# Kernel optimization log

Hardware: AMD Instinct MI355X
Metric: run time of the kernel (lower is better)

Reference implementation:

```python
import jax, jax.numpy as jnp
import numpy as np

K, M_EMB, N_HID, D_CTX, D_ATT, M_COV = 128, 256, 256, 684, 512, 256
B, H, W = 64, 16, 48


def gru_cell(x, h, W_ih, W_hh, b_ih, b_hh):
    # PyTorch GRUCell semantics
    gi = x @ W_ih.T + b_ih
    gh = h @ W_hh.T + b_hh
    i_r, i_z, i_n = jnp.split(gi, 3, axis=-1)
    h_r, h_z, h_n = jnp.split(gh, 3, axis=-1)
    r = jax.nn.sigmoid(i_r + h_r)
    z = jax.nn.sigmoid(i_z + h_z)
    n = jnp.tanh(i_n + r * h_n)
    return (1.0 - z) * n + z * h


def setup_inputs() -> dict:
    key = jax.random.key(0)
    ks = jax.random.split(key, 24)
    s = 0.02
    inp = {
        'y': jax.random.randint(ks[0], (B,), 0, K),
        'y_mask': jnp.ones((B,), jnp.float32),
        'context': jax.random.normal(ks[1], (B, D_CTX, H, W), jnp.float32),
        'pre_hidden': jax.random.normal(ks[2], (B, N_HID), jnp.float32),
        'alpha_past': jax.random.uniform(ks[3], (B, H, W), jnp.float32),
        'emb': jax.random.normal(ks[4], (K + 1, M_EMB)) * s,
        'W_ih1': jax.random.normal(ks[5], (3 * N_HID, M_EMB)) * s,
        'W_hh1': jax.random.normal(ks[6], (3 * N_HID, N_HID)) * s,
        'b_ih1': jnp.zeros((3 * N_HID,)),
        'b_hh1': jnp.zeros((3 * N_HID,)),
        'conv_Ua_w': jax.random.normal(ks[7], (D_ATT, D_CTX, 1, 1)) * s,
        'conv_Ua_b': jnp.zeros((D_ATT,)),
        'Wa': jax.random.normal(ks[8], (D_ATT, N_HID)) * s,
        'conv_Q_w': jax.random.normal(ks[9], (M_COV, 1, 3, 3)) * s,
        'Uf': jax.random.normal(ks[10], (D_ATT, M_COV)) * s,
        'Uf_b': jnp.zeros((D_ATT,)),
        'va': jax.random.normal(ks[11], (1, D_ATT)) * s,
        'va_b': jnp.zeros((1,)),
        'W_ih2': jax.random.normal(ks[12], (3 * N_HID, D_CTX)) * s,
        'W_hh2': jax.random.normal(ks[13], (3 * N_HID, N_HID)) * s,
        'b_ih2': jnp.zeros((3 * N_HID,)),
        'b_hh2': jnp.zeros((3 * N_HID,)),
        'Wct': jax.random.normal(ks[14], (M_EMB, D_CTX)) * s,
        'Wct_b': jnp.zeros((M_EMB,)),
        'Wht': jax.random.normal(ks[15], (M_EMB, N_HID)) * s,
        'Wht_b': jnp.zeros((M_EMB,)),
        'W0': jax.random.normal(ks[16], (K, M_EMB // 2)) * s,
        'W0_b': jnp.zeros((K,)),
    }
    return inp


def reference(y, y_mask, context, pre_hidden, alpha_past, emb,
              W_ih1, W_hh1, b_ih1, b_hh1, conv_Ua_w, conv_Ua_b, Wa,
              conv_Q_w, Uf, Uf_b, va, va_b,
              W_ih2, W_hh2, b_ih2, b_hh2, Wct, Wct_b, Wht, Wht_b, W0, W0_b):
    embedded = emb[y]                                           # [B, m]
    s_hat = gru_cell(embedded, pre_hidden, W_ih1, W_hh1, b_ih1, b_hh1)
    s_hat = y_mask[:, None] * s_hat + (1.0 - y_mask)[:, None] * pre_hidden

    Wa_h1 = s_hat @ Wa.T                                        # [B, A]
    # 1x1 conv == channel projection, output in NHWC layout
    Ua_ctx = jnp.einsum('bdhw,ad->bhwa', context, conv_Ua_w[:, :, 0, 0]) + conv_Ua_b
    # 3x3 coverage conv over past attention map
    cover_F = jax.lax.conv_general_dilated(
        alpha_past[:, None, :, :], conv_Q_w, (1, 1), 'SAME',
        dimension_numbers=('NCHW', 'OIHW', 'NCHW'))              # [B, M, H, W]
    cover_F = jnp.transpose(cover_F, (0, 2, 3, 1))               # [B, H, W, M]
    cover_vector = cover_F @ Uf.T + Uf_b                         # [B, H, W, A]

    e_att = jnp.tanh(Ua_ctx + Wa_h1[:, None, None, :] + cover_vector)
    alpha = (e_att @ va.T + va_b)[..., 0].reshape(e_att.shape[0], -1)  # [B, H*W]
    alpha = jax.nn.softmax(alpha, axis=1)

    ct = jnp.einsum('bdp,bp->bd', context.reshape(context.shape[0], context.shape[1], -1), alpha)

    s = gru_cell(ct, s_hat, W_ih2, W_hh2, b_ih2, b_hh2)
    s = y_mask[:, None] * s + (1.0 - y_mask)[:, None] * s_hat

    logit = ct @ Wct.T + Wct_b + s @ Wht.T + Wht_b + embedded    # [B, m]
    logit = logit.reshape(logit.shape[0], -1, 2).max(axis=2)     # maxout -> [B, m/2]
    out = logit @ W0.T + W0_b                                    # [B, K]
    return out, s, alpha.reshape(alpha.shape[0], H, W)
```

## Files before the change

### kernel.cpp

```cpp
#include <hip/hip_runtime.h>
#include <hip/hip_bf16.h>
#include <math.h>

#define BB 64
#define KV 128
#define ME 256
#define NH 256
#define DC 684
#define DA 512
#define MC 256
#define HH_ 16
#define WW_ 48
#define HW_ 768
#define NS 22

typedef __attribute__((ext_vector_type(8))) short bf16x8;
typedef __attribute__((ext_vector_type(4))) float f32x4;

#define WS_G     0
#define WS_RB    (WS_G + 4608)
#define WS_EMB   (WS_RB + 32768)
#define WS_SH    (WS_EMB + 16384)
#define WS_AL    (WS_SH + 16384)
#define WS_CT    (WS_AL + 49152)
#define WS_APACK (WS_CT + 43776)
#define WS_GI    (WS_APACK + 180224)
#define WS_GH    (WS_GI + 49152)
#define WS_LG    WS_GI
#define WS_BP    (WS_GH + 49152)
#define NEED_BYTES ((size_t)441600 * 4 + (size_t)34603008 * 2)

static __device__ __forceinline__ unsigned short f2b(float v) {
    __hip_bfloat16 h = __float2bfloat16(v);
    return *reinterpret_cast<unsigned short*>(&h);
}

template <int AUX>
static __device__ __forceinline__ void gl_lds16(const unsigned short* g,
                                                unsigned short* l) {
    __builtin_amdgcn_global_load_lds(
        (const __attribute__((address_space(1))) unsigned int*)g,
        (__attribute__((address_space(3))) unsigned int*)l, 16, 0, AUX);
}

__global__ __launch_bounds__(512) void k_prep(
    const float* __restrict__ ctx, const float* __restrict__ Ua,
    const float* __restrict__ Uf, const float* __restrict__ convQ,
    const int* __restrict__ y, const float* __restrict__ emb,
    unsigned short* __restrict__ Bpack, unsigned short* __restrict__ Apack,
    float* __restrict__ G, float* __restrict__ embedded) {
    __shared__ unsigned short Ts[64 * 360];
    int bx = blockIdx.x, t = threadIdx.x;
    if (bx < 768) {
        int b = bx / 12, pt = bx % 12, p0 = pt * 64;
        int w = t >> 6, p = t & 63;
        unsigned short* dst = Bpack + (long)(b * 12 + pt) * 22 * 2048;
        for (int ch = 0; ch < 2; ch++) {
            int dbase = ch * 352;
            if (ch) __syncthreads();
#pragma unroll
            for (int iter = 0; iter < 11; iter++) {
                int d0 = dbase + iter * 32 + w * 4;
                float v0 = 0.f, v1 = 0.f, v2 = 0.f, v3 = 0.f;
                const float* src = ctx + ((long)b * DC + d0) * HW_ + p0 + p;
                if (d0 + 0 < DC) v0 = src[0];
                if (d0 + 1 < DC) v1 = src[HW_];
                if (d0 + 2 < DC) v2 = src[2 * HW_];
                if (d0 + 3 < DC) v3 = src[3 * HW_];
                unsigned u01 = (unsigned)f2b(v0) | ((unsigned)f2b(v1) << 16);
                unsigned u23 = (unsigned)f2b(v2) | ((unsigned)f2b(v3) << 16);
                *(uint2*)&Ts[p * 360 + (d0 - dbase)] = make_uint2(u01, u23);
            }
            __syncthreads();
            int so = t >> 8;
            int tt = t & 255;
            int pp = tt >> 2, slot = tt & 3;
#pragma unroll
            for (int s2 = 0; s2 < 12; s2 += 2) {
                int sl = s2 + so;
                if (sl < 11) {
                    int s = ch * 11 + sl;
                    bf16x8 v = *(const bf16x8*)&Ts[pp * 360 + sl * 32 +
                                                   ((slot ^ ((pp >> 1) & 3))
                                                    << 3)];
                    *(bf16x8*)(dst + (long)(s * 256 + tt) * 8) = v;
                }
            }
        }
    } else if (bx < 856) {
        int bi = bx - 768;
#pragma unroll
        for (int r = 0; r < 8; r++) {
            int idx = bi * 4096 + r * 512 + t;
            int e = idx & 7, slot = (idx >> 3) & 3;
            int a = (idx >> 5) & 511, s = idx >> 14;
            int d = s * 32 + ((slot ^ ((a >> 1) & 3)) << 3) + e;
            float v = (d < DC) ? Ua[a * DC + d] : 0.f;
            Apack[idx] = f2b(v);
        }
    } else if (bx < 865) {
        int idx = (bx - 856) * 512 + t;
        if (idx < DA * 9) {
            int a = idx / 9, k = idx % 9;
            float s = 0.f;
            for (int m = 0; m < MC; m++) s += Uf[a * MC + m] * convQ[m * 9 + k];
            G[idx] = s;
        }
    } else {
        int b = bx - 865;
        if (t < ME) embedded[b * ME + t] = emb[y[b] * ME + t];
    }
}

__global__ __launch_bounds__(256) void k_G(const float* __restrict__ Uf,
                                           const float* __restrict__ convQ,
                                           float* __restrict__ G) {
    int idx = blockIdx.x * 256 + threadIdx.x;
    if (idx >= DA * 9) return;
    int a = idx / 9, k = idx % 9;
    float s = 0.f;
    for (int m = 0; m < MC; m++) s += Uf[a * MC + m] * convQ[m * 9 + k];
    G[idx] = s;
}

__global__ __launch_bounds__(256) void k_prepA(const float* __restrict__ Ua,
                                               unsigned short* __restrict__ Apack) {
    int idx = blockIdx.x * 256 + threadIdx.x;
    if (idx >= NS * DA * 32) return;
    int e = idx & 7, slot = (idx >> 3) & 3;
    int a = (idx >> 5) & 511, s = idx >> 14;
    int d = s * 32 + ((slot ^ ((a >> 1) & 3)) << 3) + e;
    float v = (d < DC) ? Ua[a * DC + d] : 0.f;
    Apack[idx] = f2b(v);
}

__global__ __launch_bounds__(256) void k_emb(const int* __restrict__ y,
                                             const float* __restrict__ emb,
                                             float* __restrict__ embedded) {
    int b = blockIdx.x, t = threadIdx.x;
    embedded[b * ME + t] = emb[y[b] * ME + t];
}

__global__ __launch_bounds__(256) void k_rows256(
    const float* __restrict__ X, const float* __restrict__ W,
    const float* __restrict__ bias, const float* __restrict__ bias2,
    float* __restrict__ out, int outStride) {
    __shared__ float Xs[64 * 257];
    __shared__ float Ws[4 * 260];
    int t = threadIdx.x, w = t >> 6, lane = t & 63;
    for (int i = t; i < 64 * 256; i += 256) {
        int bb = i >> 8, k = i & 255;
        Xs[bb * 257 + k] = X[bb * 256 + k];
    }
    int r = blockIdx.x * 4 + w;
    *(f32x4*)(Ws + w * 260 + lane * 4) = *(const f32x4*)(W + r * 256 + lane * 4);
    __syncthreads();
    const float* xrow = Xs + lane * 257;
    const float* wrow = Ws + w * 260;
    float acc = 0.f;
#pragma unroll 8
    for (int k = 0; k < 256; k++) acc += wrow[k] * xrow[k];
    acc += bias[r];
    if (bias2) acc += bias2[r];
    out[lane * outStride + r] = acc;
}

__global__ __launch_bounds__(256) void k_gih1(
    const float* __restrict__ embedded, const float* __restrict__ pre_hidden,
    const float* __restrict__ W_ih1, const float* __restrict__ W_hh1,
    const float* __restrict__ b_ih1, const float* __restrict__ b_hh1,
    float* __restrict__ gi, float* __restrict__ gh) {
    __shared__ float Xs[64 * 257];
    __shared__ float Ws[4 * 260];
    int bx = blockIdx.x, t = threadIdx.x, w = t >> 6, lane = t & 63;
    const float *X, *W, *bias;
    float* outp;
    int r;
    if (bx < 192) {
        X = embedded; W = W_ih1; bias = b_ih1; outp = gi; r = bx * 4 + w;
    } else {
        X = pre_hidden; W = W_hh1; bias = b_hh1; outp = gh; r = (bx - 192) * 4 + w;
    }
    for (int i = t; i < 64 * 256; i += 256) {
        int bb = i >> 8, k = i & 255;
        Xs[bb * 257 + k] = X[bb * 256 + k];
    }
    *(f32x4*)(Ws + w * 260 + lane * 4) = *(const f32x4*)(W + r * 256 + lane * 4);
    __syncthreads();
    const float* xrow = Xs + lane * 257;
    const float* wrow = Ws + w * 260;
    float acc = 0.f;
#pragma unroll 8
    for (int k = 0; k < 256; k++) acc += wrow[k] * xrow[k];
    outp[lane * 768 + r] = acc + bias[r];
}

__global__ __launch_bounds__(256) void k_gih2(
    const float* __restrict__ ctv, const float* __restrict__ s_hat,
    const float* __restrict__ W_ih2, const float* __restrict__ W_hh2,
    const float* __restrict__ b_ih2, const float* __restrict__ b_hh2,
    float* __restrict__ gi, float* __restrict__ gh) {
    __shared__ float Xs[64 * 257];
    __shared__ float Ws[4 * 260];
    int bx = blockIdx.x, t = threadIdx.x, w = t >> 6, lane = t & 63;
    if (bx < 192) {
        int r = bx * 4 + w;
        float acc = 0.f;
        for (int c = 0; c < 3; c++) {
            int c0 = c * 228;
            __syncthreads();
            for (int i = t; i < 64 * 228; i += 256) {
                int bb = i / 228, kk = i - bb * 228;
                Xs[bb * 229 + kk] = ctv[bb * DC + c0 + kk];
            }
            for (int j = lane; j < 228; j += 64)
                Ws[w * 260 + j] = W_ih2[r * DC + c0 + j];
            __syncthreads();
            const float* xrow = Xs + lane * 229;
            const float* wrow = Ws + w * 260;
#pragma unroll 4
            for (int k = 0; k < 228; k++) acc += wrow[k] * xrow[k];
        }
        gi[lane * 768 + r] = acc + b_ih2[r];
    } else {
        int r = (bx - 192) * 4 + w;
        for (int i = t; i < 64 * 256; i += 256) {
            int bb = i >> 8, k = i & 255;
            Xs[bb * 257 + k] = s_hat[bb * 256 + k];
        }
        *(f32x4*)(Ws + w * 260 + lane * 4) =
            *(const f32x4*)(W_hh2 + r * 256 + lane * 4);
        __syncthreads();
        const float* xrow = Xs + lane * 257;
        const float* wrow = Ws + w * 260;
        float acc = 0.f;
#pragma unroll 8
        for (int k = 0; k < 256; k++) acc += wrow[k] * xrow[k];
        gh[lane * 768 + r] = acc + b_hh2[r];
    }
}

__global__ __launch_bounds__(256) void k_gru(const float* __restrict__ gi,
                                             const float* __restrict__ gh,
                                             const float* __restrict__ h,
                                             const float* __restrict__ y_mask,
                                             float* __restrict__ outp) {
    int b = blockIdx.x, t = threadIdx.x;
    float hv = h[b * NH + t];
    float r = 1.f / (1.f + expf(-(gi[b * 768 + t] + gh[b * 768 + t])));
    float z = 1.f / (1.f + expf(-(gi[b * 768 + 256 + t] + gh[b * 768 + 256 + t])));
    float n = tanhf(gi[b * 768 + 512 + t] + r * gh[b * 768 + 512 + t]);
    float sv = (1.f - z) * n + z * hv;
    float m = y_mask[b];
    outp[b * NH + t] = m * sv + (1.f - m) * hv;
}

__global__ __launch_bounds__(512) void k_att_cnt(
    const unsigned short* __restrict__ Apack,
    const unsigned short* __restrict__ Bpack, const float* __restrict__ G,
    const float* __restrict__ rb, const float* __restrict__ va,
    const float* __restrict__ va_b, const float* __restrict__ apast,
    float* __restrict__ alogit) {
    __shared__ __attribute__((aligned(16))) unsigned short lsA[2][16384];
    __shared__ __attribute__((aligned(16))) unsigned short lsB[2][2048];
    __shared__ float ap_s[18 * 50];
    __shared__ float part_s[8][64];
    int pt = blockIdx.x, b = blockIdx.y;
    int t = threadIdx.x, w = t >> 6, lane = t & 63;
    int l15 = lane & 15, lg = lane >> 4;
    int sx = lg ^ ((l15 >> 1) & 3);

    for (int idx = t; idx < 900; idx += 512) {
        int hh = idx / 50, ww = idx % 50;
        float v = 0.f;
        if (hh >= 1 && hh <= HH_ && ww >= 1 && ww <= WW_)
            v = apast[b * HW_ + (hh - 1) * WW_ + (ww - 1)];
        ap_s[idx] = v;
    }
    __syncthreads();

    const unsigned short* Asrc = Apack + w * 2048 + lane * 8;
    const unsigned short* Bsrc =
        Bpack + (long)(b * 12 + pt) * 22 * 2048 + (w & 3) * 512 + lane * 8;

#define STAGE(S, BUF)                                                        \
    do {                                                                     \
        _Pragma("unroll") for (int i_ = 0; i_ < 4; i_++)                     \
            gl_lds16<0>(Asrc + (long)(S)*16384 + i_ * 512,                   \
                        &lsA[BUF][w * 2048 + i_ * 512]);                     \
        gl_lds16<2>(Bsrc + (long)(S)*2048, &lsB[BUF][(w & 3) * 512]);        \
    } while (0)

#define STEP_BODY(CUR)                                                       \
    do {                                                                     \
        bf16x8 af[4], bf[4];                                                 \
        _Pragma("unroll") for (int j = 0; j < 4; j++)                        \
            bf[j] = *(const bf16x8*)&lsB[CUR][(j * 16 + l15) * 32 + sx * 8]; \
        _Pragma("unroll") for (int i = 0; i < 4; i++)                        \
            af[i] = *(const bf16x8*)&lsA[CUR][(w * 64 + i * 16 + l15) * 32 + \
                                             sx * 8];                        \
        _Pragma("unroll") for (int i = 0; i < 4; i++)                        \
            _Pragma("unroll") for (int j = 0; j < 4; j++)                    \
                acc[i][j] = __builtin_amdgcn_mfma_f32_16x16x32_bf16(         \
                    af[i], bf[j], acc[i][j], 0, 0, 0);                       \
    } while (0)

    f32x4 acc[4][4];
#pragma unroll
    for (int i = 0; i < 4; i++)
#pragma unroll
        for (int j = 0; j < 4; j++) acc[i][j] = {0.f, 0.f, 0.f, 0.f};

    STAGE(0, 0);
    STAGE(1, 1);

    for (int s = 0; s < NS - 1; s++) {
        int cur = s & 1;
        asm volatile("s_waitcnt vmcnt(5)" ::: "memory");
        __builtin_amdgcn_sched_barrier(0);
        __builtin_amdgcn_s_barrier();
        __builtin_amdgcn_sched_barrier(0);
        STEP_BODY(cur);
        __builtin_amdgcn_s_barrier();
        __builtin_amdgcn_sched_barrier(0);
        if (s + 2 < NS) STAGE(s + 2, cur);
    }
    asm volatile("s_waitcnt vmcnt(0)" ::: "memory");
    __builtin_amdgcn_sched_barrier(0);
    __builtin_amdgcn_s_barrier();
    __builtin_amdgcn_sched_barrier(0);
    STEP_BODY((NS - 1) & 1);
#undef STAGE
#undef STEP_BODY

    float partial[4] = {0.f, 0.f, 0.f, 0.f};
#pragma unroll
    for (int i = 0; i < 4; i++) {
#pragma unroll
        for (int r = 0; r < 4; r++) {
            int a = w * 64 + i * 16 + lg * 4 + r;
            float rbv = rb[b * DA + a];
            float vav = va[a];
            const float* Ga = G + a * 9;
            float g0 = Ga[0], g1 = Ga[1], g2 = Ga[2], g3 = Ga[3], g4 = Ga[4];
            float g5 = Ga[5], g6 = Ga[6], g7 = Ga[7], g8 = Ga[8];
#pragma unroll
            for (int j = 0; j < 4; j++) {
                int p = pt * 64 + j * 16 + l15;
                int hh = p / WW_, ww = p % WW_;
                const float* ap = ap_s + hh * 50 + ww;
                float cov = g0 * ap[0] + g1 * ap[1] + g2 * ap[2] +
                            g3 * ap[50] + g4 * ap[51] + g5 * ap[52] +
                            g6 * ap[100] + g7 * ap[101] + g8 * ap[102];
                float e = tanhf(acc[i][j][r] + rbv + cov);
                partial[j] += vav * e;
            }
        }
    }
#pragma unroll
    for (int j = 0; j < 4; j++) {
        partial[j] += __shfl_xor(partial[j], 16);
        partial[j] += __shfl_xor(partial[j], 32);
    }
    if (lane < 16) {
#pragma unroll
        for (int j = 0; j < 4; j++) part_s[w][j * 16 + lane] = partial[j];
    }
    __syncthreads();
    if (t < 64) {
        float sum = va_b[0];
#pragma unroll
        for (int q = 0; q < 8; q++) sum += part_s[q][t];
        alogit[b * HW_ + pt * 64 + t] = sum;
    }
}

#define LDW 40
__global__ __launch_bounds__(256) void k_att_lds(
    const unsigned short* __restrict__ Apack, const float* __restrict__ ctx,
    const float* __restrict__ G, const float* __restrict__ rb,
    const float* __restrict__ va, const float* __restrict__ va_b,
    const float* __restrict__ apast, float* __restrict__ alogit) {
    __shared__ __attribute__((aligned(16))) short lsB[2][64 * LDW];
    __shared__ float ap_s[18 * 50];
    __shared__ float part_s[4 * 64];
    int b = blockIdx.y;
    int p0 = blockIdx.x * 64;
    int t = threadIdx.x;
    int w = t >> 6, lane = t & 63;
    int l15 = lane & 15, lg = lane >> 4;
    int sxA = lg ^ ((l15 >> 1) & 3);
    int pq = t & 15, kp = t >> 4;
    const float* ctx_b = ctx + (long)b * DC * HW_ + p0;

    for (int idx = t; idx < 900; idx += 256) {
        int hh = idx / 50, ww = idx % 50;
        float v = 0.f;
        if (hh >= 1 && hh <= HH_ && ww >= 1 && ww <= WW_)
            v = apast[b * HW_ + (hh - 1) * WW_ + (ww - 1)];
        ap_s[idx] = v;
    }

#define CTXLOAD(FA, FB, S)                                                   \
    do {                                                                     \
        int d_ = (S) * 32 + 2 * kp;                                          \
        const float* s0_ = ctx_b + (long)d_ * HW_ + pq;                      \
        bool g0_ = d_ < DC, g1_ = (d_ + 1) < DC;                             \
        _Pragma("unroll") for (int j_ = 0; j_ < 4; j_++) {                   \
            FA[j_] = g0_ ? s0_[16 * j_] : 0.f;                               \
            FB[j_] = g1_ ? s0_[HW_ + 16 * j_] : 0.f;                         \
        }                                                                    \
    } while (0)
#define STAGEW(FA, FB, BUF)                                                  \
    do {                                                                     \
        _Pragma("unroll") for (int j_ = 0; j_ < 4; j_++) {                   \
            ((unsigned*)lsB[BUF])[(pq + 16 * j_) * (LDW / 2) + kp] =         \
                (unsigned)f2b(FA[j_]) | ((unsigned)f2b(FB[j_]) << 16);       \
        }                                                                    \
    } while (0)
#define ALOAD(AF, S)                                                         \
    do {                                                                     \
        _Pragma("unroll") for (int i_ = 0; i_ < 8; i_++)                     \
            AF[i_] = *(const bf16x8*)(Apack +                                \
                ((long)((S)*512 + w * 128 + i_ * 16 + l15) * 4 + sxA) * 8);  \
    } while (0)
#define BREAD(BF, BUF)                                                       \
    do {                                                                     \
        _Pragma("unroll") for (int j_ = 0; j_ < 4; j_++)                     \
            BF[j_] = *(const bf16x8*)(&lsB[BUF][(j_ * 16 + l15) * LDW +      \
                                               lg * 8]);                     \
    } while (0)
#define MFMA8x4(AF, BF)                                                      \
    do {                                                                     \
        _Pragma("unroll") for (int i_ = 0; i_ < 8; i_++)                     \
            _Pragma("unroll") for (int j_ = 0; j_ < 4; j_++)                 \
                acc[i_][j_] = __builtin_amdgcn_mfma_f32_16x16x32_bf16(       \
                    AF[i_], BF[j_], acc[i_][j_], 0, 0, 0);                   \
    } while (0)

    f32x4 acc[8][4];
#pragma unroll
    for (int i = 0; i < 8; i++)
#pragma unroll
        for (int j = 0; j < 4; j++) acc[i][j] = {0.f, 0.f, 0.f, 0.f};

    float fa0[4], fb0[4], fa1[4], fb1[4];
    bf16x8 afr0[8], afr1[8], bfr[4];

    CTXLOAD(fa1, fb1, 0);
    ALOAD(afr0, 0);
    STAGEW(fa1, fb1, 0);
    CTXLOAD(fa1, fb1, 1);
    __syncthreads();

    for (int ss = 0; ss < NS; ss += 2) {
        if (ss + 2 < NS) CTXLOAD(fa0, fb0, ss + 2);
        ALOAD(afr1, ss + 1);
        BREAD(bfr, 0);
        STAGEW(fa1, fb1, 1);
        MFMA8x4(afr0, bfr);
        __syncthreads();
        if (ss + 3 < NS) CTXLOAD(fa1, fb1, ss + 3);
        if (ss + 2 < NS) {
            ALOAD(afr0, ss + 2);
            BREAD(bfr, 1);
            STAGEW(fa0, fb0, 0);
            MFMA8x4(afr1, bfr);
        } else {
            BREAD(bfr, 1);
            MFMA8x4(afr1, bfr);
        }
        __syncthreads();
    }

    float partial[4] = {0.f, 0.f, 0.f, 0.f};
#pragma unroll
    for (int i = 0; i < 8; i++) {
#pragma unroll
        for (int r = 0; r < 4; r++) {
            int a = w * 128 + i * 16 + lg * 4 + r;
            float rbv = rb[b * DA + a];
            float vav = va[a];
            const float* Ga = G + a * 9;
            float g0 = Ga[0], g1 = Ga[1], g2 = Ga[2], g3 = Ga[3], g4 = Ga[4];
            float g5 = Ga[5], g6 = Ga[6], g7 = Ga[7], g8 = Ga[8];
#pragma unroll
            for (int j = 0; j < 4; j++) {
                int p = p0 + j * 16 + l15;
                int hh = p / WW_, ww = p % WW_;
                const float* ap = ap_s + hh * 50 + ww;
                float cov = g0 * ap[0] + g1 * ap[1] + g2 * ap[2] +
                            g3 * ap[50] + g4 * ap[51] + g5 * ap[52] +
                            g6 * ap[100] + g7 * ap[101] + g8 * ap[102];
                float e = tanhf(acc[i][j][r] + rbv + cov);
                partial[j] += vav * e;
            }
        }
    }
#pragma unroll
    for (int j = 0; j < 4; j++) {
        partial[j] += __shfl_xor(partial[j], 16);
        partial[j] += __shfl_xor(partial[j], 32);
    }
    if (lane < 16) {
#pragma unroll
        for (int j = 0; j < 4; j++) part_s[w * 64 + j * 16 + lane] = partial[j];
    }
    __syncthreads();
    if (t < 64) {
        float s = va_b[0] + part_s[t] + part_s[64 + t] + part_s[128 + t] +
                  part_s[192 + t];
        alogit[b * HW_ + p0 + t] = s;
    }
}

__global__ __launch_bounds__(256) void k_ctsm(const float* __restrict__ ctx,
                                              const float* __restrict__ alogit,
                                              float* __restrict__ ct,
                                              float* __restrict__ alpha_out) {
    __shared__ float al_s[HW_];
    __shared__ float red[16];
    int b = blockIdx.y, t = threadIdx.x;
    float v[3];
    float mx = -1e30f;
    for (int i = 0; i < 3; i++) {
        v[i] = alogit[b * HW_ + i * 256 + t];
        mx = fmaxf(mx, v[i]);
    }
    for (int off = 32; off > 0; off >>= 1) mx = fmaxf(mx, __shfl_down(mx, off));
    if ((t & 63) == 0) red[t >> 6] = mx;
    __syncthreads();
    if (t == 0) red[0] = fmaxf(fmaxf(red[0], red[1]), fmaxf(red[2], red[3]));
    __syncthreads();
    mx = red[0];
    float sum = 0.f;
    for (int i = 0; i < 3; i++) {
        v[i] = expf(v[i] - mx);
        sum += v[i];
    }
    for (int off = 32; off > 0; off >>= 1) sum += __shfl_down(sum, off);
    if ((t & 63) == 0) red[8 + (t >> 6)] = sum;
    __syncthreads();
    if (t == 0) red[8] = red[8] + red[9] + red[10] + red[11];
    __syncthreads();
    float inv = 1.f / red[8];
    for (int i = 0; i < 3; i++) {
        float a = v[i] * inv;
        al_s[i * 256 + t] = a;
        if (blockIdx.x == 0) alpha_out[b * HW_ + i * 256 + t] = a;
    }
    __syncthreads();
    int dc0 = blockIdx.x * 114;
    int wave = t >> 6, lane = t & 63;
    for (int d = dc0 + wave; d < dc0 + 114; d += 4) {
        const float* row = &ctx[((long)b * DC + d) * HW_];
        float s = 0.f;
#pragma unroll
        for (int q = 0; q < 12; q++) s += row[lane + q * 64] * al_s[lane + q * 64];
        for (int off = 32; off > 0; off >>= 1) s += __shfl_down(s, off);
        if (lane == 0) ct[b * DC + d] = s;
    }
}

__global__ __launch_bounds__(256) void k_logit(
    const float* __restrict__ ctv, const float* __restrict__ s,
    const float* __restrict__ embedded, const float* __restrict__ Wct,
    const float* __restrict__ Wht, const float* __restrict__ Wct_b,
    const float* __restrict__ Wht_b, float* __restrict__ lg) {
    __shared__ float Xs[64 * 257];
    __shared__ float Ws[4 * 232];
    int t = threadIdx.x, w = t >> 6, lane = t & 63;
    int r = blockIdx.x * 4 + w;
    float acc = 0.f;
    for (int c = 0; c < 3; c++) {
        int c0 = c * 228;
        __syncthreads();
        for (int i = t; i < 64 * 228; i += 256) {
            int bb = i / 228, kk = i - bb * 228;
            Xs[bb * 229 + kk] = ctv[bb * DC + c0 + kk];
        }
        for (int j = lane; j < 228; j += 64) Ws[w * 232 + j] = Wct[r * DC + c0 + j];
        __syncthreads();
        const float* xrow = Xs + lane * 229;
        const float* wrow = Ws + w * 232;
#pragma unroll 4
        for (int k = 0; k < 228; k++) acc += wrow[k] * xrow[k];
    }
    __syncthreads();
    for (int i = t; i < 64 * 256; i += 256) {
        int bb = i >> 8, k = i & 255;
        Xs[bb * 257 + k] = s[bb * 256 + k];
    }
    __syncthreads();
    const float* xrow2 = Xs + lane * 257;
    const float* wr = Wht + r * 256;
    float acc2 = 0.f;
#pragma unroll 8
    for (int k = 0; k < 256; k++) acc2 += wr[k] * xrow2[k];
    lg[lane * 256 + r] = acc + acc2 + Wct_b[r] + Wht_b[r] + embedded[lane * 256 + r];
}

__global__ __launch_bounds__(256) void k_head(const float* __restrict__ lg,
                                              const float* __restrict__ W0,
                                              const float* __restrict__ W0_b,
                                              float* __restrict__ out) {
    __shared__ float Xs[64 * 129];
    __shared__ float Ws[4 * 132];
    int t = threadIdx.x, w = t >> 6, lane = t & 63;
    for (int i = t; i < 64 * 128; i += 256) {
        int bb = i >> 7, m = i & 127;
        Xs[bb * 129 + m] = fmaxf(lg[bb * 256 + 2 * m], lg[bb * 256 + 2 * m + 1]);
    }
    int r = blockIdx.x * 4 + w;
    Ws[w * 132 + lane] = W0[r * 128 + lane];
    Ws[w * 132 + 64 + lane] = W0[r * 128 + 64 + lane];
    __syncthreads();
    const float* xrow = Xs + lane * 129;
    const float* wrow = Ws + w * 132;
    float acc = 0.f;
#pragma unroll 8
    for (int k = 0; k < 128; k++) acc += wrow[k] * xrow[k];
    out[lane * KV + r] = acc + W0_b[r];
}

extern "C" void kernel_launch(void* const* d_in, const int* in_sizes, int n_in,
                              void* d_out, int out_size, void* d_ws,
                              size_t ws_size, hipStream_t stream) {
    const int* y = (const int*)d_in[0];
    const float* y_mask = (const float*)d_in[1];
    const float* context = (const float*)d_in[2];
    const float* pre_hidden = (const float*)d_in[3];
    const float* alpha_past = (const float*)d_in[4];
    const float* emb = (const float*)d_in[5];
    const float* W_ih1 = (const float*)d_in[6];
    const float* W_hh1 = (const float*)d_in[7];
    const float* b_ih1 = (const float*)d_in[8];
    const float* b_hh1 = (const float*)d_in[9];
    const float* conv_Ua_w = (const float*)d_in[10];
    const float* conv_Ua_b = (const float*)d_in[11];
    const float* Wa = (const float*)d_in[12];
    const float* conv_Q_w = (const float*)d_in[13];
    const float* Uf = (const float*)d_in[14];
    const float* Uf_b = (const float*)d_in[15];
    const float* va = (const float*)d_in[16];
    const float* va_b = (const float*)d_in[17];
    const float* W_ih2 = (const float*)d_in[18];
    const float* W_hh2 = (const float*)d_in[19];
    const float* b_ih2 = (const float*)d_in[20];
    const float* b_hh2 = (const float*)d_in[21];
    const float* Wct = (const float*)d_in[22];
    const float* Wct_b = (const float*)d_in[23];
    const float* Wht = (const float*)d_in[24];
    const float* Wht_b = (const float*)d_in[25];
    const float* W0 = (const float*)d_in[26];
    const float* W0_b = (const float*)d_in[27];

    float* ws = (float*)d_ws;
    float* out = (float*)d_out;
    float* G = ws + WS_G;
    float* rbias = ws + WS_RB;
    float* embedded = ws + WS_EMB;
    float* s_hat = ws + WS_SH;
    float* alogit = ws + WS_AL;
    float* ctv = ws + WS_CT;
    unsigned short* Apack = (unsigned short*)(ws + WS_APACK);
    float* gi = ws + WS_GI;
    float* gh = ws + WS_GH;
    float* lg = ws + WS_LG;
    unsigned short* Bpack = (unsigned short*)(ws + WS_BP);
    float* s_out = out + 8192;
    float* alpha_out = out + 24576;

    bool fast = ws_size >= NEED_BYTES;

    if (fast) {
        k_prep<<<dim3(929), dim3(512), 0, stream>>>(context, conv_Ua_w, Uf,
                                                    conv_Q_w, y, emb, Bpack,
                                                    Apack, G, embedded);
    } else {
        k_G<<<dim3(18), dim3(256), 0, stream>>>(Uf, conv_Q_w, G);
        k_prepA<<<dim3((NS * DA * 32 + 255) / 256), dim3(256), 0, stream>>>(
            conv_Ua_w, Apack);
        k_emb<<<dim3(64), dim3(256), 0, stream>>>(y, emb, embedded);
    }
    k_gih1<<<dim3(384), dim3(256), 0, stream>>>(embedded, pre_hidden, W_ih1,
                                                W_hh1, b_ih1, b_hh1, gi, gh);
    k_gru<<<dim3(64), dim3(256), 0, stream>>>(gi, gh, pre_hidden, y_mask, s_hat);
    k_rows256<<<dim3(128), dim3(256), 0, stream>>>(s_hat, Wa, conv_Ua_b, Uf_b,
                                                   rbias, 512);
    if (fast) {
        k_att_cnt<<<dim3(12, 64), dim3(512), 0, stream>>>(
            Apack, Bpack, G, rbias, va, va_b, alpha_past, alogit);
    } else {
        k_att_lds<<<dim3(12, 64), dim3(256), 0, stream>>>(
            Apack, context, G, rbias, va, va_b, alpha_past, alogit);
    }
    k_ctsm<<<dim3(6, 64), dim3(256), 0, stream>>>(context, alogit, ctv,
                                                  alpha_out);
    k_gih2<<<dim3(384), dim3(256), 0, stream>>>(ctv, s_hat, W_ih2, W_hh2, b_ih2,
                                                b_hh2, gi, gh);
    k_gru<<<dim3(64), dim3(256), 0, stream>>>(gi, gh, s_hat, y_mask, s_out);
    k_logit<<<dim3(64), dim3(256), 0, stream>>>(ctv, s_out, embedded, Wct, Wht,
                                                Wct_b, Wht_b, lg);
    k_head<<<dim3(32), dim3(256), 0, stream>>>(lg, W0, W0_b, out);
}
```

Before: 247.6 us.

## Retile attention GEMM into 256x192 blocks split over attention-dim halves

The attention-energy kernel now tiles each block as half of the attention dimension (256) by 192 positions instead of all 512 by 64, so each wave computes a 64x96 output tile with six B fragments per step. This raises A-operand reuse across positions and cuts repeated loads of the packed Ua weights, at the cost of two partial logit buffers that the softmax kernel sums. The va_b bias is dropped because softmax is shift-invariant. The fallback path zeroes the second buffer with a memset, and the larger accumulator array raises register pressure.

```diff
diff --git a/kernel.cpp b/kernel.cpp
--- a/kernel.cpp
+++ b/kernel.cpp
@@ -28,7 +28,8 @@
 #define WS_GH    (WS_GI + 49152)
 #define WS_LG    WS_GI
 #define WS_BP    (WS_GH + 49152)
-#define NEED_BYTES ((size_t)441600 * 4 + (size_t)34603008 * 2)
+#define WS_AL2   (WS_BP + 17301504)
+#define NEED_BYTES ((size_t)(441600 + 17301504 + 49152) * 4)
 
 static __device__ __forceinline__ unsigned short f2b(float v) {
     __hip_bfloat16 h = __float2bfloat16(v);
@@ -255,19 +256,20 @@
     outp[b * NH + t] = m * sv + (1.f - m) * hv;
 }
 
-__global__ __launch_bounds__(512) void k_att_cnt(
+__global__ __launch_bounds__(512) void k_att3(
     const unsigned short* __restrict__ Apack,
     const unsigned short* __restrict__ Bpack, const float* __restrict__ G,
     const float* __restrict__ rb, const float* __restrict__ va,
-    const float* __restrict__ va_b, const float* __restrict__ apast,
-    float* __restrict__ alogit) {
-    __shared__ __attribute__((aligned(16))) unsigned short lsA[2][16384];
-    __shared__ __attribute__((aligned(16))) unsigned short lsB[2][2048];
+    const float* __restrict__ apast, float* __restrict__ alogit0,
+    float* __restrict__ alogit1) {
+    __shared__ __attribute__((aligned(16))) unsigned short lsA[2][8192];
+    __shared__ __attribute__((aligned(16))) unsigned short lsB[2][6144];
     __shared__ float ap_s[18 * 50];
-    __shared__ float part_s[8][64];
-    int pt = blockIdx.x, b = blockIdx.y;
+    __shared__ float part_s[8][96];
+    int pt = blockIdx.x, ah = blockIdx.y, b = blockIdx.z;
     int t = threadIdx.x, w = t >> 6, lane = t & 63;
     int l15 = lane & 15, lg = lane >> 4;
+    int aw = w & 3, pw = w >> 2;
     int sx = lg ^ ((l15 >> 1) & 3);
 
     for (int idx = t; idx < 900; idx += 512) {
@@ -279,44 +281,57 @@
     }
     __syncthreads();
 
-    const unsigned short* Asrc = Apack + w * 2048 + lane * 8;
-    const unsigned short* Bsrc =
-        Bpack + (long)(b * 12 + pt) * 22 * 2048 + (w & 3) * 512 + lane * 8;
+    const unsigned short* Ap0 = Apack + ah * 8192 + w * 1024 + lane * 8;
+    const unsigned short* Bp0[2];
+    int ldst[2];
+    {
+#pragma unroll
+        for (int i = 0; i < 2; i++) {
+            int l = w * 2 + i;
+            if (l >= 12) l -= 12;
+            int c = l >> 2, q = l & 3;
+            Bp0[i] = Bpack + (long)(b * 12 + pt * 3 + c) * 22 * 2048 + q * 512 +
+                     lane * 8;
+            ldst[i] = c * 2048 + q * 512;
+        }
+    }
 
 #define STAGE(S, BUF)                                                        \
     do {                                                                     \
-        _Pragma("unroll") for (int i_ = 0; i_ < 4; i_++)                     \
-            gl_lds16<0>(Asrc + (long)(S)*16384 + i_ * 512,                   \
-                        &lsA[BUF][w * 2048 + i_ * 512]);                     \
-        gl_lds16<2>(Bsrc + (long)(S)*2048, &lsB[BUF][(w & 3) * 512]);        \
+        _Pragma("unroll") for (int i_ = 0; i_ < 2; i_++)                     \
+            gl_lds16<0>(Ap0 + (long)(S)*16384 + i_ * 512,                    \
+                        &lsA[BUF][w * 1024 + i_ * 512]);                     \
+        _Pragma("unroll") for (int i_ = 0; i_ < 2; i_++)                     \
+            gl_lds16<2>(Bp0[i_] + (long)(S)*2048, &lsB[BUF][ldst[i_]]);      \
     } while (0)
 
 #define STEP_BODY(CUR)                                                       \
     do {                                                                     \
-        bf16x8 af[4], bf[4];                                                 \
-        _Pragma("unroll") for (int j = 0; j < 4; j++)                        \
-            bf[j] = *(const bf16x8*)&lsB[CUR][(j * 16 + l15) * 32 + sx * 8]; \
+        bf16x8 af[4], bf[6];                                                 \
         _Pragma("unroll") for (int i = 0; i < 4; i++)                        \
-            af[i] = *(const bf16x8*)&lsA[CUR][(w * 64 + i * 16 + l15) * 32 + \
+            af[i] = *(const bf16x8*)&lsA[CUR][(aw * 64 + i * 16 + l15) * 32 +\
+                                             sx * 8];                        \
+        _Pragma("unroll") for (int j = 0; j < 6; j++)                        \
+            bf[j] = *(const bf16x8*)&lsB[CUR][(pw * 96 + j * 16 + l15) * 32 +\
                                              sx * 8];                        \
         _Pragma("unroll") for (int i = 0; i < 4; i++)                        \
-            _Pragma("unroll") for (int j = 0; j < 4; j++)                    \
+            _Pragma("unroll") for (int j = 0; j < 6; j++)                    \
                 acc[i][j] = __builtin_amdgcn_mfma_f32_16x16x32_bf16(         \
                     af[i], bf[j], acc[i][j], 0, 0, 0);                       \
     } while (0)
 
-    f32x4 acc[4][4];
+    f32x4 acc[4][6];
 #pragma unroll
     for (int i = 0; i < 4; i++)
 #pragma unroll
-        for (int j = 0; j < 4; j++) acc[i][j] = {0.f, 0.f, 0.f, 0.f};
+        for (int j = 0; j < 6; j++) acc[i][j] = {0.f, 0.f, 0.f, 0.f};
 
     STAGE(0, 0);
     STAGE(1, 1);
 
     for (int s = 0; s < NS - 1; s++) {
         int cur = s & 1;
-        asm volatile("s_waitcnt vmcnt(5)" ::: "memory");
+        asm volatile("s_waitcnt vmcnt(4)" ::: "memory");
         __builtin_amdgcn_sched_barrier(0);
         __builtin_amdgcn_s_barrier();
         __builtin_amdgcn_sched_barrier(0);
@@ -333,20 +348,20 @@
 #undef STAGE
 #undef STEP_BODY
 
-    float partial[4] = {0.f, 0.f, 0.f, 0.f};
+    float partial[6] = {0.f, 0.f, 0.f, 0.f, 0.f, 0.f};
 #pragma unroll
     for (int i = 0; i < 4; i++) {
 #pragma unroll
         for (int r = 0; r < 4; r++) {
-            int a = w * 64 + i * 16 + lg * 4 + r;
+            int a = ah * 256 + aw * 64 + i * 16 + lg * 4 + r;
             float rbv = rb[b * DA + a];
             float vav = va[a];
             const float* Ga = G + a * 9;
             float g0 = Ga[0], g1 = Ga[1], g2 = Ga[2], g3 = Ga[3], g4 = Ga[4];
             float g5 = Ga[5], g6 = Ga[6], g7 = Ga[7], g8 = Ga[8];
 #pragma unroll
-            for (int j = 0; j < 4; j++) {
-                int p = pt * 64 + j * 16 + l15;
+            for (int j = 0; j < 6; j++) {
+                int p = pt * 192 + pw * 96 + j * 16 + l15;
                 int hh = p / WW_, ww = p % WW_;
                 const float* ap = ap_s + hh * 50 + ww;
                 float cov = g0 * ap[0] + g1 * ap[1] + g2 * ap[2] +
@@ -358,20 +373,21 @@
         }
     }
 #pragma unroll
-    for (int j = 0; j < 4; j++) {
+    for (int j = 0; j < 6; j++) {
         partial[j] += __shfl_xor(partial[j], 16);
         partial[j] += __shfl_xor(partial[j], 32);
     }
     if (lane < 16) {
 #pragma unroll
-        for (int j = 0; j < 4; j++) part_s[w][j * 16 + lane] = partial[j];
-    }
-    __syncthreads();
-    if (t < 64) {
-        float sum = va_b[0];
-#pragma unroll
-        for (int q = 0; q < 8; q++) sum += part_s[q][t];
-        alogit[b * HW_ + pt * 64 + t] = sum;
+        for (int j = 0; j < 6; j++) part_s[w][j * 16 + lane] = partial[j];
+    }
+    __syncthreads();
+    if (t < 192) {
+        int pg = t / 96, pl = t % 96;
+        float sum = part_s[pg * 4 + 0][pl] + part_s[pg * 4 + 1][pl] +
+                    part_s[pg * 4 + 2][pl] + part_s[pg * 4 + 3][pl];
+        float* dst = ah ? alogit1 : alogit0;
+        dst[b * HW_ + pt * 192 + t] = sum;
     }
 }
 
@@ -379,8 +395,8 @@
 __global__ __launch_bounds__(256) void k_att_lds(
     const unsigned short* __restrict__ Apack, const float* __restrict__ ctx,
     const float* __restrict__ G, const float* __restrict__ rb,
-    const float* __restrict__ va, const float* __restrict__ va_b,
-    const float* __restrict__ apast, float* __restrict__ alogit) {
+    const float* __restrict__ va, const float* __restrict__ apast,
+    float* __restrict__ alogit) {
     __shared__ __attribute__((aligned(16))) short lsB[2][64 * LDW];
     __shared__ float ap_s[18 * 50];
     __shared__ float part_s[4 * 64];
@@ -508,14 +524,15 @@
     }
     __syncthreads();
     if (t < 64) {
-        float s = va_b[0] + part_s[t] + part_s[64 + t] + part_s[128 + t] +
+        float s = part_s[t] + part_s[64 + t] + part_s[128 + t] +
                   part_s[192 + t];
         alogit[b * HW_ + p0 + t] = s;
     }
 }
 
 __global__ __launch_bounds__(256) void k_ctsm(const float* __restrict__ ctx,
-                                              const float* __restrict__ alogit,
+                                              const float* __restrict__ alogit0,
+                                              const float* __restrict__ alogit1,
                                               float* __restrict__ ct,
                                               float* __restrict__ alpha_out) {
     __shared__ float al_s[HW_];
@@ -524,7 +541,8 @@
     float v[3];
     float mx = -1e30f;
     for (int i = 0; i < 3; i++) {
-        v[i] = alogit[b * HW_ + i * 256 + t];
+        int idx = b * HW_ + i * 256 + t;
+        v[i] = alogit0[idx] + alogit1[idx];
         mx = fmaxf(mx, v[i]);
     }
     for (int off = 32; off > 0; off >>= 1) mx = fmaxf(mx, __shfl_down(mx, off));
@@ -668,6 +686,7 @@
     float* gh = ws + WS_GH;
     float* lg = ws + WS_LG;
     unsigned short* Bpack = (unsigned short*)(ws + WS_BP);
+    float* alogit2 = ws + WS_AL2;
     float* s_out = out + 8192;
     float* alpha_out = out + 24576;
 
@@ -682,6 +701,7 @@
         k_prepA<<<dim3((NS * DA * 32 + 255) / 256), dim3(256), 0, stream>>>(
             conv_Ua_w, Apack);
         k_emb<<<dim3(64), dim3(256), 0, stream>>>(y, emb, embedded);
+        hipMemsetAsync(alogit2, 0, 49152 * sizeof(float), stream);
     }
     k_gih1<<<dim3(384), dim3(256), 0, stream>>>(embedded, pre_hidden, W_ih1,
                                                 W_hh1, b_ih1, b_hh1, gi, gh);
@@ -689,14 +709,14 @@
     k_rows256<<<dim3(128), dim3(256), 0, stream>>>(s_hat, Wa, conv_Ua_b, Uf_b,
                                                    rbias, 512);
     if (fast) {
-        k_att_cnt<<<dim3(12, 64), dim3(512), 0, stream>>>(
-            Apack, Bpack, G, rbias, va, va_b, alpha_past, alogit);
+        k_att3<<<dim3(4, 2, 64), dim3(512), 0, stream>>>(
+            Apack, Bpack, G, rbias, va, alpha_past, alogit, alogit2);
     } else {
         k_att_lds<<<dim3(12, 64), dim3(256), 0, stream>>>(
-            Apack, context, G, rbias, va, va_b, alpha_past, alogit);
-    }
-    k_ctsm<<<dim3(6, 64), dim3(256), 0, stream>>>(context, alogit, ctv,
-                                                  alpha_out);
+            Apack, context, G, rbias, va, alpha_past, alogit);
+    }
+    k_ctsm<<<dim3(6, 64), dim3(256), 0, stream>>>(context, alogit, alogit2,
+                                                  ctv, alpha_out);
     k_gih2<<<dim3(384), dim3(256), 0, stream>>>(ctv, s_hat, W_ih2, W_hh2, b_ih2,
                                                 b_hh2, gi, gh);
     k_gru<<<dim3(64), dim3(256), 0, stream>>>(gi, gh, s_hat, y_mask, s_out);
```

Result: slower. 254.9 us (+2.9%).
